# Performance work log

Measured on AMD Instinct MI355X. Metric: run time of the kernel, lower is better.

Reference implementation:

```python
import jax, jax.numpy as jnp
import numpy as np

LN_EPS = 1e-5

def layer_norm(x, g, b):
    mu = jnp.mean(x, axis=-1, keepdims=True)
    var = jnp.var(x, axis=-1, keepdims=True)
    return (x - mu) * jax.lax.rsqrt(var + LN_EPS) * g + b

def setup_inputs() -> dict:
    key = jax.random.key(0)
    ks = jax.random.split(key, 4)
    d = 2048
    bs, win_len, obj_num = 8, 64, 36
    return {
        "visual_feats": jax.random.normal(ks[0], (bs, win_len, d), dtype=jnp.float32),
        "obj_feats": jax.random.normal(ks[1], (bs, win_len, obj_num, d), dtype=jnp.float32),
        "W_v": jax.random.normal(ks[2], (d, d), dtype=jnp.float32) * (1.0 / np.sqrt(d)),
        "b_v": jnp.zeros((d,), dtype=jnp.float32),
        "W_o": jax.random.normal(ks[3], (d, d), dtype=jnp.float32) * (1.0 / np.sqrt(d)),
        "b_o": jnp.zeros((d,), dtype=jnp.float32),
        "ln_v_g": jnp.ones((d,), dtype=jnp.float32),
        "ln_v_b": jnp.zeros((d,), dtype=jnp.float32),
        "ln_o_g": jnp.ones((d,), dtype=jnp.float32),
        "ln_o_b": jnp.zeros((d,), dtype=jnp.float32),
        "ln_ov_g": jnp.ones((d,), dtype=jnp.float32),
        "ln_ov_b": jnp.zeros((d,), dtype=jnp.float32),
    }

def reference(visual_feats, obj_feats, W_v, b_v, W_o, b_o,
              ln_v_g, ln_v_b, ln_o_g, ln_o_b, ln_ov_g, ln_ov_b):
    bs, win_len, obj_num, obj_size = obj_feats.shape
    # visual branch: linear -> tanh -> LN   [bs, F, d]
    ve = layer_norm(jnp.tanh(visual_feats @ W_v + b_v), ln_v_g, ln_v_b)
    # object branch: linear -> flatten frames*objects -> tanh -> LN  [bs, N, d]
    oe = (obj_feats @ W_o + b_o).reshape(bs, win_len * obj_num, obj_size)
    oe = layer_norm(jnp.tanh(oe), ln_o_g, ln_o_b)
    # adjacency: [bs, N, F], softmax over N (object axis, dim=1)
    adj = jnp.einsum('bnd,bfd->bnf', oe, ve) / jnp.sqrt(jnp.asarray(obj_size, dtype=oe.dtype))
    adj = jax.nn.softmax(adj, axis=1)
    # aggregate objects per frame: (oe^T @ adj)^T -> [bs, F, d]
    obj_agg = jnp.einsum('bnd,bnf->bfd', oe, adj)
    return layer_norm(jnp.tanh(obj_agg + ve), ln_ov_g, ln_ov_b)
```

## Files before the change

### kernel.cpp

```cpp
#include <hip/hip_runtime.h>
#include <cstdint>
#include <cstddef>


typedef __attribute__((ext_vector_type(4))) float f32x4;
typedef __attribute__((ext_vector_type(4))) unsigned int u32x4;
typedef __attribute__((ext_vector_type(8))) short bf16x8;

#define DD 2048
#define BS 8
#define FF 64
#define NOBJ 2304
#define MO 18432
#define MV 512

__device__ __forceinline__ unsigned short f2bf(float f) {
  unsigned int u = __float_as_uint(f);
  u += 0x7fffu + ((u >> 16) & 1u);
  return (unsigned short)(u >> 16);
}
__device__ __forceinline__ unsigned int pk2(float a, float b) {
  return (unsigned int)f2bf(a) | ((unsigned int)f2bf(b) << 16);
}
__device__ __forceinline__ float bf2f(unsigned short u) {
  return __uint_as_float((unsigned int)u << 16);
}

typedef __attribute__((address_space(1))) const unsigned int gas_u32;
typedef __attribute__((address_space(3))) unsigned int las_u32;
__device__ __forceinline__ void gl_lds16(const void* g, void* l) {
  __builtin_amdgcn_global_load_lds((gas_u32*)g, (las_u32*)l, 16, 0, 0);
}

__global__ __launch_bounds__(256) void k_cvt_bf16(const float* __restrict__ X,
                                                  unsigned short* __restrict__ O,
                                                  int n16) {
  int idx = blockIdx.x * 256 + threadIdx.x;
  const int stride = gridDim.x * 256;
  for (int i = idx; i < n16; i += stride) {
    const f32x4* src = (const f32x4*)(X + (size_t)i * 16);
    f32x4 a = src[0], b = src[1], c = src[2], d = src[3];
    u32x4 p = {pk2(a.x, a.y), pk2(a.z, a.w), pk2(b.x, b.y), pk2(b.z, b.w)};
    u32x4 q = {pk2(c.x, c.y), pk2(c.z, c.w), pk2(d.x, d.y), pk2(d.z, d.w)};
    u32x4* dst = (u32x4*)(O + (size_t)i * 16);
    dst[0] = p;
    dst[1] = q;
  }
}

__global__ __launch_bounds__(256) void k_wprep2(const float* __restrict__ Wv,
                                                const float* __restrict__ Wo,
                                                unsigned short* __restrict__ WvT,
                                                unsigned short* __restrict__ WoT) {
  __shared__ unsigned short sh[64][65];
  const float* W = blockIdx.z ? Wo : Wv;
  unsigned short* Wt = blockIdx.z ? WoT : WvT;
  const int t = threadIdx.x;
  const int kb = blockIdx.x * 64, nb = blockIdx.y * 64;
  {
    const int rk = t >> 2, seg = t & 3;
    const float* src = W + (size_t)(kb + rk) * DD + nb + seg * 16;
#pragma unroll
    for (int q = 0; q < 4; ++q) {
      f32x4 x = *(const f32x4*)(src + q * 4);
      sh[rk][seg * 16 + q * 4 + 0] = f2bf(x.x);
      sh[rk][seg * 16 + q * 4 + 1] = f2bf(x.y);
      sh[rk][seg * 16 + q * 4 + 2] = f2bf(x.z);
      sh[rk][seg * 16 + q * 4 + 3] = f2bf(x.w);
    }
  }
  __syncthreads();
  {
    const int nn = t >> 2, ks = t & 3;
    unsigned int o[8];
#pragma unroll
    for (int j = 0; j < 8; ++j)
      o[j] = (unsigned int)sh[ks * 16 + 2 * j][nn] |
             ((unsigned int)sh[ks * 16 + 2 * j + 1][nn] << 16);
    u32x4 p0 = {o[0], o[1], o[2], o[3]};
    u32x4 p1 = {o[4], o[5], o[6], o[7]};
    unsigned short* dst = Wt + (size_t)(nb + nn) * DD + kb + ks * 16;
    ((u32x4*)dst)[0] = p0;
    ((u32x4*)dst)[1] = p1;
  }
}

__global__ __launch_bounds__(512, 1) void k_gemm_bbf(const unsigned short* __restrict__ A,
                                                     const unsigned short* __restrict__ Bt,
                                                     const float* __restrict__ bias,
                                                     unsigned short* __restrict__ T,
                                                     float* __restrict__ part) {
  __shared__ __align__(16) unsigned short lds[3 * 24576];
  const int tid = threadIdx.x;
  const int lane = tid & 63, wave = tid >> 6;
  const int r = lane & 15, g = lane >> 4;
  const int wm = wave >> 1, wn = wave & 1;

  const int orig = blockIdx.y * 16 + blockIdx.x;
  const int lin = (orig & 7) * 144 + (orig >> 3);
  const int bm = (lin >> 4) * 256;
  const int bn = (lin & 15) * 128;

  const int srow = tid >> 3;
  const int k16s = (tid & 7) ^ (srow & 7);
  const unsigned short* aSrc[4];
#pragma unroll
  for (int q = 0; q < 4; ++q)
    aSrc[q] = A + (size_t)(bm + q * 64 + srow) * DD + k16s * 8;
  const unsigned short* bSrc[2];
#pragma unroll
  for (int q = 0; q < 2; ++q)
    bSrc[q] = Bt + (size_t)(bn + q * 64 + srow) * DD + k16s * 8;

  auto stage = [&](int buf, int kt) {
    unsigned short* ab = lds + buf * 24576;
    unsigned short* bb = ab + 16384;
    const size_t ko = (size_t)kt * 64;
#pragma unroll
    for (int q = 0; q < 4; ++q)
      gl_lds16(aSrc[q] + ko, ab + ((q * 512 + tid) << 3));
#pragma unroll
    for (int q = 0; q < 2; ++q)
      gl_lds16(bSrc[q] + ko, bb + ((q * 512 + tid) << 3));
  };

  const int rs = r & 7;
  const int sa0 = ((0 + g) ^ rs) * 8;
  const int sa1 = ((4 + g) ^ rs) * 8;
  const int arow0 = wm * 64 + r;
  const int brow0 = wn * 64 + r;

  f32x4 acc[4][4] = {};
  stage(0, 0);
  stage(1, 1);
  asm volatile("s_waitcnt vmcnt(6)" ::: "memory");
  __builtin_amdgcn_s_barrier();

  for (int kt = 0; kt < DD / 64; ++kt) {
    const int cur = kt % 3;
    if (kt + 2 < DD / 64) stage((kt + 2) % 3, kt + 2);
    const unsigned short* ab = lds + cur * 24576;
    const unsigned short* bb = ab + 16384;
    bf16x8 af[4][2], bfr[4][2];
#pragma unroll
    for (int mi = 0; mi < 4; ++mi) {
      const int ro = (arow0 + mi * 16) * 64;
      af[mi][0] = *(const bf16x8*)(ab + ro + sa0);
      af[mi][1] = *(const bf16x8*)(ab + ro + sa1);
    }
#pragma unroll
    for (int ni = 0; ni < 4; ++ni) {
      const int ro = (brow0 + ni * 16) * 64;
      bfr[ni][0] = *(const bf16x8*)(bb + ro + sa0);
      bfr[ni][1] = *(const bf16x8*)(bb + ro + sa1);
    }
    __builtin_amdgcn_s_setprio(1);
#pragma unroll
    for (int mi = 0; mi < 4; ++mi)
#pragma unroll
      for (int ni = 0; ni < 4; ++ni) {
        acc[mi][ni] = __builtin_amdgcn_mfma_f32_16x16x32_bf16(af[mi][0], bfr[ni][0], acc[mi][ni], 0, 0, 0);
        acc[mi][ni] = __builtin_amdgcn_mfma_f32_16x16x32_bf16(af[mi][1], bfr[ni][1], acc[mi][ni], 0, 0, 0);
      }
    __builtin_amdgcn_s_setprio(0);
    if (kt < DD / 64 - 2) {
      asm volatile("s_waitcnt vmcnt(6)" ::: "memory");
    } else {
      asm volatile("s_waitcnt vmcnt(0)" ::: "memory");
    }
    __builtin_amdgcn_s_barrier();
  }

  float bv[4];
#pragma unroll
  for (int ni = 0; ni < 4; ++ni) bv[ni] = bias[bn + wn * 64 + ni * 16 + r];
  const int slot = ((lin & 15) << 1) + wn;
#pragma unroll
  for (int mi = 0; mi < 4; ++mi) {
#pragma unroll
    for (int i2 = 0; i2 < 4; ++i2) {
      const int row = bm + wm * 64 + mi * 16 + g * 4 + i2;
      unsigned short* trow = T + (size_t)row * DD + bn + wn * 64 + r;
      float s1 = 0.f, s2 = 0.f;
#pragma unroll
      for (int ni = 0; ni < 4; ++ni) {
        const float tv = tanhf(acc[mi][ni][i2] + bv[ni]);
        trow[ni * 16] = f2bf(tv);
        s1 += tv;
        s2 += tv * tv;
      }
#pragma unroll
      for (int m = 1; m < 16; m <<= 1) {
        s1 += __shfl_xor(s1, m, 64);
        s2 += __shfl_xor(s2, m, 64);
      }
      if (r == 0) {
        float2 p2 = make_float2(s1, s2);
        *(float2*)(part + (size_t)row * 64 + slot * 2) = p2;
      }
    }
  }
}

__global__ __launch_bounds__(256) void k_stats(const float* __restrict__ part,
                                               float2* __restrict__ stats) {
  const int t = threadIdx.x;
  const int row = blockIdx.x * 8 + (t >> 5);
  const int i = t & 31;
  float2 p = ((const float2*)(part + (size_t)row * 64))[i];
  float s1 = p.x, s2 = p.y;
#pragma unroll
  for (int m = 1; m < 32; m <<= 1) {
    s1 += __shfl_xor(s1, m, 64);
    s2 += __shfl_xor(s2, m, 64);
  }
  if (i == 0) {
    const float mean = s1 * (1.0f / DD);
    const float var = s2 * (1.0f / DD) - mean * mean;
    stats[row] = make_float2(mean, rsqrtf(var + 1e-5f));
  }
}

__global__ __launch_bounds__(256) void k_lnT(const unsigned short* __restrict__ T,
                                             const float2* __restrict__ stats,
                                             const float* __restrict__ gw,
                                             const float* __restrict__ bw,
                                             unsigned short* __restrict__ oe,
                                             unsigned short* __restrict__ oeT) {
  __shared__ unsigned short sh[64][65];
  const int t = threadIdx.x;
  const int b = blockIdx.z, nt = blockIdx.x, dt = blockIdx.y;
  {
    const int nn = t >> 2, seg = t & 3;
    const int row = b * NOBJ + nt * 64 + nn;
    const size_t base = (size_t)row * DD + dt * 64 + seg * 16;
    u32x4 x0 = ((const u32x4*)(T + base))[0];
    u32x4 x1 = ((const u32x4*)(T + base))[1];
    const float2 st = stats[row];
    const float* gp = gw + dt * 64 + seg * 16;
    const float* bp = bw + dt * 64 + seg * 16;
    f32x4 gq[4], bq[4];
#pragma unroll
    for (int q = 0; q < 4; ++q) {
      gq[q] = ((const f32x4*)gp)[q];
      bq[q] = ((const f32x4*)bp)[q];
    }
    const unsigned short* px0 = (const unsigned short*)&x0;
    const unsigned short* px1 = (const unsigned short*)&x1;
    unsigned short ov[16];
#pragma unroll
    for (int j = 0; j < 8; ++j) {
      const float v = bf2f(px0[j]);
      ov[j] = f2bf((v - st.x) * st.y * gq[j >> 2][j & 3] + bq[j >> 2][j & 3]);
    }
#pragma unroll
    for (int j = 0; j < 8; ++j) {
      const float v = bf2f(px1[j]);
      ov[8 + j] = f2bf((v - st.x) * st.y * gq[2 + (j >> 2)][j & 3] + bq[2 + (j >> 2)][j & 3]);
    }
    u32x4 o0 = {(unsigned int)ov[0] | ((unsigned int)ov[1] << 16),
                (unsigned int)ov[2] | ((unsigned int)ov[3] << 16),
                (unsigned int)ov[4] | ((unsigned int)ov[5] << 16),
                (unsigned int)ov[6] | ((unsigned int)ov[7] << 16)};
    u32x4 o1 = {(unsigned int)ov[8] | ((unsigned int)ov[9] << 16),
                (unsigned int)ov[10] | ((unsigned int)ov[11] << 16),
                (unsigned int)ov[12] | ((unsigned int)ov[13] << 16),
                (unsigned int)ov[14] | ((unsigned int)ov[15] << 16)};
    ((u32x4*)(oe + base))[0] = o0;
    ((u32x4*)(oe + base))[1] = o1;
#pragma unroll
    for (int j = 0; j < 16; ++j) sh[nn][seg * 16 + j] = ov[j];
  }
  __syncthreads();
  {
    const int dd = t >> 2, ns = t & 3;
    unsigned int o[8];
#pragma unroll
    for (int j = 0; j < 8; ++j)
      o[j] = (unsigned int)sh[ns * 16 + 2 * j][dd] |
             ((unsigned int)sh[ns * 16 + 2 * j + 1][dd] << 16);
    u32x4 p0 = {o[0], o[1], o[2], o[3]};
    u32x4 p1 = {o[4], o[5], o[6], o[7]};
    unsigned short* dst = oeT + ((size_t)b * DD + dt * 64 + dd) * NOBJ + nt * 64 + ns * 16;
    ((u32x4*)dst)[0] = p0;
    ((u32x4*)dst)[1] = p1;
  }
}

__global__ __launch_bounds__(256) void k_gemm_xw(const float* __restrict__ X,
                                                 const unsigned short* __restrict__ Wt,
                                                 const float* __restrict__ bias,
                                                 float* __restrict__ Y) {
  __shared__ __align__(16) unsigned short As[128 * 32];
  __shared__ __align__(16) unsigned short Bs[128 * 32];
  const int t = threadIdx.x;
  const int lane = t & 63, wave = t >> 6;
  const int r = lane & 15, g = lane >> 4;
  const int wm = wave >> 1, wn = wave & 1;
  const int bm = blockIdx.y * 128, bn = blockIdx.x * 128;
  const int arow = t >> 1, ah = t & 1;
  f32x4 acc[4][4] = {};
  const float* aptr = X + (size_t)(bm + arow) * DD + ah * 16;
  const unsigned short* bptr = Wt + (size_t)(bn + arow) * DD + ah * 16;
  for (int kt = 0; kt < DD / 32; ++kt) {
    const int kb = kt * 32;
    f32x4 a0 = *(const f32x4*)(aptr + kb);
    f32x4 a1 = *(const f32x4*)(aptr + kb + 4);
    f32x4 a2 = *(const f32x4*)(aptr + kb + 8);
    f32x4 a3 = *(const f32x4*)(aptr + kb + 12);
    u32x4 b0 = *(const u32x4*)(bptr + kb);
    u32x4 b1 = *(const u32x4*)(bptr + kb + 8);
    __syncthreads();
    u32x4 p0 = {pk2(a0.x, a0.y), pk2(a0.z, a0.w), pk2(a1.x, a1.y), pk2(a1.z, a1.w)};
    u32x4 p1 = {pk2(a2.x, a2.y), pk2(a2.z, a2.w), pk2(a3.x, a3.y), pk2(a3.z, a3.w)};
    ((u32x4*)As)[arow * 4 + ah * 2 + 0] = p0;
    ((u32x4*)As)[arow * 4 + ah * 2 + 1] = p1;
    ((u32x4*)Bs)[arow * 4 + ah * 2 + 0] = b0;
    ((u32x4*)Bs)[arow * 4 + ah * 2 + 1] = b1;
    __syncthreads();
    bf16x8 af[4], bfr[4];
#pragma unroll
    for (int m = 0; m < 4; ++m) af[m] = ((const bf16x8*)As)[(wm * 64 + m * 16 + r) * 4 + g];
#pragma unroll
    for (int n = 0; n < 4; ++n) bfr[n] = ((const bf16x8*)Bs)[(wn * 64 + n * 16 + r) * 4 + g];
#pragma unroll
    for (int m = 0; m < 4; ++m)
#pragma unroll
      for (int n = 0; n < 4; ++n)
        acc[m][n] = __builtin_amdgcn_mfma_f32_16x16x32_bf16(af[m], bfr[n], acc[m][n], 0, 0, 0);
  }
#pragma unroll
  for (int m = 0; m < 4; ++m) {
    const int row0 = bm + wm * 64 + m * 16 + g * 4;
#pragma unroll
    for (int n = 0; n < 4; ++n) {
      const int col = bn + wn * 64 + n * 16 + r;
      const float bvx = bias[col];
#pragma unroll
      for (int i = 0; i < 4; ++i)
        Y[(size_t)(row0 + i) * DD + col] = acc[m][n][i] + bvx;
    }
  }
}

__global__ __launch_bounds__(256) void k_ep_ln(const float* __restrict__ Y,
                                               const float* __restrict__ Y2,
                                               const float* __restrict__ gw,
                                               const float* __restrict__ bw,
                                               unsigned short* __restrict__ obf,
                                               float* __restrict__ of32) {
  const int row = blockIdx.x, t = threadIdx.x;
  const size_t base = (size_t)row * DD + t * 8;
  f32x4 v0 = ((const f32x4*)(Y + base))[0];
  f32x4 v1 = ((const f32x4*)(Y + base))[1];
  if (Y2 != nullptr) {
    v0 += ((const f32x4*)(Y2 + base))[0];
    v1 += ((const f32x4*)(Y2 + base))[1];
  }
  float tv[8];
#pragma unroll
  for (int j = 0; j < 4; ++j) {
    tv[j] = tanhf(v0[j]);
    tv[4 + j] = tanhf(v1[j]);
  }
  float s1 = 0.f, s2 = 0.f;
#pragma unroll
  for (int j = 0; j < 8; ++j) {
    s1 += tv[j];
    s2 += tv[j] * tv[j];
  }
#pragma unroll
  for (int m = 1; m < 64; m <<= 1) {
    s1 += __shfl_xor(s1, m, 64);
    s2 += __shfl_xor(s2, m, 64);
  }
  __shared__ float r1[4], r2[4];
  const int wave = t >> 6;
  if ((t & 63) == 0) {
    r1[wave] = s1;
    r2[wave] = s2;
  }
  __syncthreads();
  const float S1 = r1[0] + r1[1] + r1[2] + r1[3];
  const float S2 = r2[0] + r2[1] + r2[2] + r2[3];
  const float mean = S1 * (1.0f / DD);
  const float var = S2 * (1.0f / DD) - mean * mean;
  const float rstd = rsqrtf(var + 1e-5f);
  f32x4 g0 = ((const f32x4*)(gw + t * 8))[0], g1 = ((const f32x4*)(gw + t * 8))[1];
  f32x4 bb0 = ((const f32x4*)(bw + t * 8))[0], bb1 = ((const f32x4*)(bw + t * 8))[1];
  float o[8];
#pragma unroll
  for (int j = 0; j < 4; ++j) {
    o[j] = (tv[j] - mean) * rstd * g0[j] + bb0[j];
    o[4 + j] = (tv[4 + j] - mean) * rstd * g1[j] + bb1[j];
  }
  if (obf != nullptr) {
    u32x4 p = {pk2(o[0], o[1]), pk2(o[2], o[3]), pk2(o[4], o[5]), pk2(o[6], o[7])};
    *((u32x4*)(obf + base)) = p;
  }
  if (of32 != nullptr) {
    f32x4 w0 = {o[0], o[1], o[2], o[3]}, w1 = {o[4], o[5], o[6], o[7]};
    ((f32x4*)(of32 + base))[0] = w0;
    ((f32x4*)(of32 + base))[1] = w1;
  }
}

__global__ __launch_bounds__(256) void k_gemm_adj(const unsigned short* __restrict__ oe,
                                                  const unsigned short* __restrict__ veb,
                                                  float* __restrict__ adjT) {
  __shared__ __align__(16) unsigned short As[64 * 32];
  __shared__ __align__(16) unsigned short Bs[64 * 32];
  const int t = threadIdx.x;
  const int lane = t & 63, wave = t >> 6;
  const int r = lane & 15, g = lane >> 4;
  const int wm = wave >> 1, wn = wave & 1;
  const int b = blockIdx.y, bm = blockIdx.x * 64;
  const int arow = t >> 2, aseg = t & 3;
  f32x4 acc[2][2] = {};
  const unsigned short* aptr = oe + ((size_t)b * NOBJ + bm + arow) * DD + aseg * 8;
  const unsigned short* bptr = veb + ((size_t)b * FF + arow) * DD + aseg * 8;
  for (int kt = 0; kt < DD / 32; ++kt) {
    const int kb = kt * 32;
    u32x4 a0 = *(const u32x4*)(aptr + kb);
    u32x4 bvx = *(const u32x4*)(bptr + kb);
    __syncthreads();
    ((u32x4*)As)[arow * 4 + aseg] = a0;
    ((u32x4*)Bs)[arow * 4 + aseg] = bvx;
    __syncthreads();
    bf16x8 af[2], bfr[2];
#pragma unroll
    for (int m = 0; m < 2; ++m) af[m] = ((const bf16x8*)As)[(wm * 32 + m * 16 + r) * 4 + g];
#pragma unroll
    for (int n = 0; n < 2; ++n) bfr[n] = ((const bf16x8*)Bs)[(wn * 32 + n * 16 + r) * 4 + g];
#pragma unroll
    for (int m = 0; m < 2; ++m)
#pragma unroll
      for (int n = 0; n < 2; ++n)
        acc[m][n] = __builtin_amdgcn_mfma_f32_16x16x32_bf16(af[m], bfr[n], acc[m][n], 0, 0, 0);
  }
  const float scale = 0.02209708691207961f;
#pragma unroll
  for (int m = 0; m < 2; ++m)
#pragma unroll
    for (int n = 0; n < 2; ++n) {
      const int f = wn * 32 + n * 16 + r;
      const int n0 = bm + wm * 32 + m * 16 + g * 4;
      f32x4 v = acc[m][n];
      v *= scale;
      *(f32x4*)(adjT + ((size_t)b * FF + f) * NOBJ + n0) = v;
    }
}

__global__ __launch_bounds__(256) void k_smax(const float* __restrict__ adjT,
                                              unsigned short* __restrict__ out) {
  const int t = threadIdx.x;
  const size_t base = (size_t)blockIdx.x * NOBJ;
  float v[9];
#pragma unroll
  for (int j = 0; j < 9; ++j) v[j] = adjT[base + t + j * 256];
  float m = v[0];
#pragma unroll
  for (int j = 1; j < 9; ++j) m = fmaxf(m, v[j]);
#pragma unroll
  for (int s = 1; s < 64; s <<= 1) m = fmaxf(m, __shfl_xor(m, s, 64));
  __shared__ float rm[4], rs[4];
  const int wave = t >> 6;
  if ((t & 63) == 0) rm[wave] = m;
  __syncthreads();
  m = fmaxf(fmaxf(rm[0], rm[1]), fmaxf(rm[2], rm[3]));
  float e[9];
  float s = 0.f;
#pragma unroll
  for (int j = 0; j < 9; ++j) {
    e[j] = __expf(v[j] - m);
    s += e[j];
  }
#pragma unroll
  for (int q = 1; q < 64; q <<= 1) s += __shfl_xor(s, q, 64);
  if ((t & 63) == 0) rs[wave] = s;
  __syncthreads();
  const float S = rs[0] + rs[1] + rs[2] + rs[3];
  const float inv = 1.0f / S;
#pragma unroll
  for (int j = 0; j < 9; ++j) out[base + t + j * 256] = f2bf(e[j] * inv);
}

__global__ __launch_bounds__(256) void k_gemm_agg(const unsigned short* __restrict__ adjsm,
                                                  const unsigned short* __restrict__ oeT,
                                                  float* __restrict__ agg) {
  __shared__ __align__(16) unsigned short As[64 * 32];
  __shared__ __align__(16) unsigned short Bs[64 * 32];
  const int t = threadIdx.x;
  const int lane = t & 63, wave = t >> 6;
  const int r = lane & 15, g = lane >> 4;
  const int wm = wave >> 1, wn = wave & 1;
  const int b = blockIdx.y, bn = blockIdx.x * 64;
  const int arow = t >> 2, aseg = t & 3;
  f32x4 acc[2][2] = {};
  const unsigned short* aptr = adjsm + ((size_t)b * FF + arow) * NOBJ + aseg * 8;
  const unsigned short* bptr = oeT + ((size_t)b * DD + bn + arow) * NOBJ + aseg * 8;
  for (int kt = 0; kt < NOBJ / 32; ++kt) {
    const int kb = kt * 32;
    u32x4 av = *(const u32x4*)(aptr + kb);
    u32x4 bvx = *(const u32x4*)(bptr + kb);
    __syncthreads();
    ((u32x4*)As)[arow * 4 + aseg] = av;
    ((u32x4*)Bs)[arow * 4 + aseg] = bvx;
    __syncthreads();
    bf16x8 af[2], bfr[2];
#pragma unroll
    for (int m = 0; m < 2; ++m) af[m] = ((const bf16x8*)As)[(wm * 32 + m * 16 + r) * 4 + g];
#pragma unroll
    for (int n = 0; n < 2; ++n) bfr[n] = ((const bf16x8*)Bs)[(wn * 32 + n * 16 + r) * 4 + g];
#pragma unroll
    for (int m = 0; m < 2; ++m)
#pragma unroll
      for (int n = 0; n < 2; ++n)
        acc[m][n] = __builtin_amdgcn_mfma_f32_16x16x32_bf16(af[m], bfr[n], acc[m][n], 0, 0, 0);
  }
#pragma unroll
  for (int m = 0; m < 2; ++m)
#pragma unroll
    for (int n = 0; n < 2; ++n) {
      const int d = bn + wn * 32 + n * 16 + r;
#pragma unroll
      for (int i = 0; i < 4; ++i) {
        const int f = wm * 32 + m * 16 + g * 4 + i;
        agg[((size_t)b * FF + f) * DD + d] = acc[m][n][i];
      }
    }
}


extern "C" void kernel_launch(void* const* d_in, const int* in_sizes, int n_in,
                              void* d_out, int out_size, void* d_ws, size_t ws_size,
                              hipStream_t stream) {
  (void)in_sizes; (void)n_in; (void)out_size;
  const float* visual = (const float*)d_in[0];
  const float* obj    = (const float*)d_in[1];
  const float* W_v    = (const float*)d_in[2];
  const float* b_v    = (const float*)d_in[3];
  const float* W_o    = (const float*)d_in[4];
  const float* b_o    = (const float*)d_in[5];
  const float* ln_v_g = (const float*)d_in[6];
  const float* ln_v_b = (const float*)d_in[7];
  const float* ln_o_g = (const float*)d_in[8];
  const float* ln_o_b = (const float*)d_in[9];
  const float* ln_ov_g = (const float*)d_in[10];
  const float* ln_ov_b = (const float*)d_in[11];

  char* ws = (char*)d_ws;
  constexpr size_t OFF_WVT  = 0;
  constexpr size_t OFF_ADJ  = 0;
  constexpr size_t OFF_ADJS = 5ull << 20;
  constexpr size_t OFF_WOT  = 8ull << 20;
  constexpr size_t OFF_AGG  = 8ull << 20;
  constexpr size_t OFF_OBJB = 16ull << 20;
  constexpr size_t OFF_OET  = 16ull << 20;
  constexpr size_t OFF_T    = 88ull << 20;
  constexpr size_t OFF_PART = 160ull << 20;
  constexpr size_t OFF_STAT = 165ull << 20;
  constexpr size_t OFF_YV   = 166ull << 20;
  constexpr size_t OFF_VEF  = 170ull << 20;
  constexpr size_t OFF_VEB  = 174ull << 20;
  constexpr size_t OFF_OEB  = 176ull << 20;
  constexpr size_t WS_NEED  = 248ull << 20;
  if (ws_size < WS_NEED) return;

  unsigned short* WvT  = (unsigned short*)(ws + OFF_WVT);
  unsigned short* WoT  = (unsigned short*)(ws + OFF_WOT);
  unsigned short* objb = (unsigned short*)(ws + OFF_OBJB);
  unsigned short* oeT  = (unsigned short*)(ws + OFF_OET);
  unsigned short* T    = (unsigned short*)(ws + OFF_T);
  float* part          = (float*)(ws + OFF_PART);
  float2* stats        = (float2*)(ws + OFF_STAT);
  float* Yv            = (float*)(ws + OFF_YV);
  float* ve_f          = (float*)(ws + OFF_VEF);
  unsigned short* ve_b = (unsigned short*)(ws + OFF_VEB);
  unsigned short* oe_b = (unsigned short*)(ws + OFF_OEB);
  float* adjT          = (float*)(ws + OFF_ADJ);
  unsigned short* adjs = (unsigned short*)(ws + OFF_ADJS);
  float* agg           = (float*)(ws + OFF_AGG);

  dim3 b256(256);
  k_wprep2<<<dim3(32, 32, 2), b256, 0, stream>>>(W_v, W_o, WvT, WoT);
  k_cvt_bf16<<<dim3(2048), b256, 0, stream>>>(obj, objb, MO * DD / 16);
  k_gemm_xw<<<dim3(16, MV / 128), b256, 0, stream>>>(visual, WvT, b_v, Yv);
  k_gemm_bbf<<<dim3(16, MO / 256), dim3(512), 0, stream>>>(objb, WoT, b_o, T, part);
  k_ep_ln<<<dim3(MV), b256, 0, stream>>>(Yv, nullptr, ln_v_g, ln_v_b, ve_b, ve_f);
  k_stats<<<dim3(MO / 8), b256, 0, stream>>>(part, stats);
  k_lnT<<<dim3(36, 32, 8), b256, 0, stream>>>(T, stats, ln_o_g, ln_o_b, oe_b, oeT);
  k_gemm_adj<<<dim3(NOBJ / 64, BS), b256, 0, stream>>>(oe_b, ve_b, adjT);
  k_smax<<<dim3(MV), b256, 0, stream>>>(adjT, adjs);
  k_gemm_agg<<<dim3(DD / 64, BS), b256, 0, stream>>>(adjs, oeT, agg);
  k_ep_ln<<<dim3(MV), b256, 0, stream>>>(agg, ve_f, ln_ov_g, ln_ov_b, nullptr, (float*)d_out);
}
```

Measured before the change: 454.5 us.

## Fuse fp32-to-bf16 conversion of object features into the object GEMM loader

Drops the separate conversion kernel that wrote a bf16 copy of the 302 MB fp32 object tensor. The GEMM now loads fp32 A tiles into registers, converts them to bf16, and writes them to LDS itself. B tiles still go through direct global-to-LDS loads. This removes a full write and re-read of the bf16 copy, but A is now staged through registers. The loop also waits with vmcnt(0) every iteration, which may expose more load latency, and each A tile is re-read in fp32 by all 16 column blocks, doubling A traffic through L2.

```diff
diff --git a/kernel.cpp b/kernel.cpp
--- a/kernel.cpp
+++ b/kernel.cpp
@@ -1,4 +1,5 @@
 #include <hip/hip_runtime.h>
+#include <hip/hip_bf16.h>
 #include <cstdint>
 #include <cstddef>
 
@@ -25,27 +26,15 @@
 __device__ __forceinline__ float bf2f(unsigned short u) {
   return __uint_as_float((unsigned int)u << 16);
 }
+__device__ __forceinline__ unsigned int pkrn(float a, float b) {
+  __hip_bfloat162 h = __float22bfloat162_rn(make_float2(a, b));
+  return *reinterpret_cast<unsigned int*>(&h);
+}
 
 typedef __attribute__((address_space(1))) const unsigned int gas_u32;
 typedef __attribute__((address_space(3))) unsigned int las_u32;
 __device__ __forceinline__ void gl_lds16(const void* g, void* l) {
   __builtin_amdgcn_global_load_lds((gas_u32*)g, (las_u32*)l, 16, 0, 0);
-}
-
-__global__ __launch_bounds__(256) void k_cvt_bf16(const float* __restrict__ X,
-                                                  unsigned short* __restrict__ O,
-                                                  int n16) {
-  int idx = blockIdx.x * 256 + threadIdx.x;
-  const int stride = gridDim.x * 256;
-  for (int i = idx; i < n16; i += stride) {
-    const f32x4* src = (const f32x4*)(X + (size_t)i * 16);
-    f32x4 a = src[0], b = src[1], c = src[2], d = src[3];
-    u32x4 p = {pk2(a.x, a.y), pk2(a.z, a.w), pk2(b.x, b.y), pk2(b.z, b.w)};
-    u32x4 q = {pk2(c.x, c.y), pk2(c.z, c.w), pk2(d.x, d.y), pk2(d.z, d.w)};
-    u32x4* dst = (u32x4*)(O + (size_t)i * 16);
-    dst[0] = p;
-    dst[1] = q;
-  }
 }
 
 __global__ __launch_bounds__(256) void k_wprep2(const float* __restrict__ Wv,
@@ -85,7 +74,7 @@
   }
 }
 
-__global__ __launch_bounds__(512, 1) void k_gemm_bbf(const unsigned short* __restrict__ A,
+__global__ __launch_bounds__(512, 1) void k_gemm_bbf(const float* __restrict__ A32,
                                                      const unsigned short* __restrict__ Bt,
                                                      const float* __restrict__ bias,
                                                      unsigned short* __restrict__ T,
@@ -103,25 +92,37 @@
 
   const int srow = tid >> 3;
   const int k16s = (tid & 7) ^ (srow & 7);
-  const unsigned short* aSrc[4];
+  const float* aSrc[4];
 #pragma unroll
   for (int q = 0; q < 4; ++q)
-    aSrc[q] = A + (size_t)(bm + q * 64 + srow) * DD + k16s * 8;
+    aSrc[q] = A32 + (size_t)(bm + q * 64 + srow) * DD + k16s * 8;
   const unsigned short* bSrc[2];
 #pragma unroll
   for (int q = 0; q < 2; ++q)
     bSrc[q] = Bt + (size_t)(bn + q * 64 + srow) * DD + k16s * 8;
 
-  auto stage = [&](int buf, int kt) {
-    unsigned short* ab = lds + buf * 24576;
-    unsigned short* bb = ab + 16384;
+  f32x4 aR[4][2];
+
+  auto stageIssue = [&](int buf, int kt) {
     const size_t ko = (size_t)kt * 64;
 #pragma unroll
-    for (int q = 0; q < 4; ++q)
-      gl_lds16(aSrc[q] + ko, ab + ((q * 512 + tid) << 3));
+    for (int q = 0; q < 4; ++q) {
+      aR[q][0] = ((const f32x4*)(aSrc[q] + ko))[0];
+      aR[q][1] = ((const f32x4*)(aSrc[q] + ko))[1];
+    }
+    unsigned short* bb = lds + buf * 24576 + 16384;
 #pragma unroll
     for (int q = 0; q < 2; ++q)
       gl_lds16(bSrc[q] + ko, bb + ((q * 512 + tid) << 3));
+  };
+  auto stageWrite = [&](int buf) {
+    unsigned short* ab = lds + buf * 24576;
+#pragma unroll
+    for (int q = 0; q < 4; ++q) {
+      u32x4 w = {pkrn(aR[q][0].x, aR[q][0].y), pkrn(aR[q][0].z, aR[q][0].w),
+                 pkrn(aR[q][1].x, aR[q][1].y), pkrn(aR[q][1].z, aR[q][1].w)};
+      *(u32x4*)(ab + ((q * 512 + tid) << 3)) = w;
+    }
   };
 
   const int rs = r & 7;
@@ -131,14 +132,19 @@
   const int brow0 = wn * 64 + r;
 
   f32x4 acc[4][4] = {};
-  stage(0, 0);
-  stage(1, 1);
-  asm volatile("s_waitcnt vmcnt(6)" ::: "memory");
+  stageIssue(0, 0);
+  asm volatile("s_waitcnt vmcnt(0)" ::: "memory");
+  stageWrite(0);
+  stageIssue(1, 1);
+  asm volatile("s_waitcnt vmcnt(0)" ::: "memory");
+  stageWrite(1);
+  asm volatile("s_waitcnt lgkmcnt(0)" ::: "memory");
   __builtin_amdgcn_s_barrier();
 
   for (int kt = 0; kt < DD / 64; ++kt) {
     const int cur = kt % 3;
-    if (kt + 2 < DD / 64) stage((kt + 2) % 3, kt + 2);
+    const bool st = (kt + 2 < DD / 64);
+    if (st) stageIssue((kt + 2) % 3, kt + 2);
     const unsigned short* ab = lds + cur * 24576;
     const unsigned short* bb = ab + 16384;
     bf16x8 af[4][2], bfr[4][2];
@@ -163,11 +169,9 @@
         acc[mi][ni] = __builtin_amdgcn_mfma_f32_16x16x32_bf16(af[mi][1], bfr[ni][1], acc[mi][ni], 0, 0, 0);
       }
     __builtin_amdgcn_s_setprio(0);
-    if (kt < DD / 64 - 2) {
-      asm volatile("s_waitcnt vmcnt(6)" ::: "memory");
-    } else {
-      asm volatile("s_waitcnt vmcnt(0)" ::: "memory");
-    }
+    asm volatile("s_waitcnt vmcnt(0)" ::: "memory");
+    if (st) stageWrite((kt + 2) % 3);
+    asm volatile("s_waitcnt lgkmcnt(0)" ::: "memory");
     __builtin_amdgcn_s_barrier();
   }
 
@@ -555,7 +559,6 @@
   constexpr size_t OFF_ADJS = 5ull << 20;
   constexpr size_t OFF_WOT  = 8ull << 20;
   constexpr size_t OFF_AGG  = 8ull << 20;
-  constexpr size_t OFF_OBJB = 16ull << 20;
   constexpr size_t OFF_OET  = 16ull << 20;
   constexpr size_t OFF_T    = 88ull << 20;
   constexpr size_t OFF_PART = 160ull << 20;
@@ -569,7 +572,6 @@
 
   unsigned short* WvT  = (unsigned short*)(ws + OFF_WVT);
   unsigned short* WoT  = (unsigned short*)(ws + OFF_WOT);
-  unsigned short* objb = (unsigned short*)(ws + OFF_OBJB);
   unsigned short* oeT  = (unsigned short*)(ws + OFF_OET);
   unsigned short* T    = (unsigned short*)(ws + OFF_T);
   float* part          = (float*)(ws + OFF_PART);
@@ -584,9 +586,8 @@
 
   dim3 b256(256);
   k_wprep2<<<dim3(32, 32, 2), b256, 0, stream>>>(W_v, W_o, WvT, WoT);
-  k_cvt_bf16<<<dim3(2048), b256, 0, stream>>>(obj, objb, MO * DD / 16);
   k_gemm_xw<<<dim3(16, MV / 128), b256, 0, stream>>>(visual, WvT, b_v, Yv);
-  k_gemm_bbf<<<dim3(16, MO / 256), dim3(512), 0, stream>>>(objb, WoT, b_o, T, part);
+  k_gemm_bbf<<<dim3(16, MO / 256), dim3(512), 0, stream>>>(obj, WoT, b_o, T, part);
   k_ep_ln<<<dim3(MV), b256, 0, stream>>>(Yv, nullptr, ln_v_g, ln_v_b, ve_b, ve_f);
   k_stats<<<dim3(MO / 8), b256, 0, stream>>>(part, stats);
   k_lnT<<<dim3(36, 32, 8), b256, 0, stream>>>(T, stats, ln_o_g, ln_o_b, oe_b, oeT);
```

New measurement: 562.0 us. 1.24x slower.
